# Kernel tuning notes

Hardware: AMD Instinct MI355X
Metric: run time of the kernel (lower is better)

## Reference

```python
import jax, jax.numpy as jnp
import numpy as np

B, S, HID = 2, 2048, 1024
NH, NKV, HD = 16, 8, 128
EPS = 1e-6
THETA = 1.0e6
NEG = -1e9

def _rope_tables():
    inv_freq = 1.0 / (THETA ** (np.arange(0, HD, 2, dtype=np.float32) / HD))  # [HD/2]
    pos = np.arange(S, dtype=np.float32)
    freqs = np.outer(pos, inv_freq)                      # [S, HD/2]
    emb = np.concatenate([freqs, freqs], axis=-1)        # [S, HD]
    cos = np.broadcast_to(np.cos(emb), (B, S, HD)).copy()
    sin = np.broadcast_to(np.sin(emb), (B, S, HD)).copy()
    return jnp.asarray(cos), jnp.asarray(sin)

def setup_inputs() -> dict:
    key = jax.random.key(0)
    ks = jax.random.split(key, 8)
    hidden_states = jax.random.normal(ks[0], (B, S, HID), jnp.float32)
    cos, sin = _rope_tables()
    # additive causal mask [B,1,S,S]
    causal = jnp.triu(jnp.full((S, S), NEG, jnp.float32), k=1)
    attention_mask = jnp.broadcast_to(causal[None, None], (B, 1, S, S))
    std = 0.02
    Wq = jax.random.normal(ks[1], (NH * HD, HID), jnp.float32) * std
    Wk = jax.random.normal(ks[2], (NKV * HD, HID), jnp.float32) * std
    Wv = jax.random.normal(ks[3], (NKV * HD, HID), jnp.float32) * std
    Wo = jax.random.normal(ks[4], (HID, NH * HD), jnp.float32) * std
    q_norm_w = jnp.ones((HD,), jnp.float32)
    k_norm_w = jnp.ones((HD,), jnp.float32)
    return {"hidden_states": hidden_states, "cos": cos, "sin": sin,
            "attention_mask": attention_mask, "Wq": Wq, "Wk": Wk, "Wv": Wv,
            "Wo": Wo, "q_norm_w": q_norm_w, "k_norm_w": k_norm_w}

def _rms_norm(x, w):
    var = jnp.mean(jnp.square(x), axis=-1, keepdims=True)
    return x * jax.lax.rsqrt(var + EPS) * w

def _rotate_half(x):
    x1, x2 = jnp.split(x, 2, axis=-1)
    return jnp.concatenate([-x2, x1], axis=-1)

def reference(hidden_states, cos, sin, attention_mask, Wq, Wk, Wv, Wo, q_norm_w, k_norm_w):
    # projections: [B,S,heads,HD] -> [B,heads,S,HD]
    q = jnp.einsum('bsh,dh->bsd', hidden_states, Wq).reshape(B, S, NH, HD)
    k = jnp.einsum('bsh,dh->bsd', hidden_states, Wk).reshape(B, S, NKV, HD)
    v = jnp.einsum('bsh,dh->bsd', hidden_states, Wv).reshape(B, S, NKV, HD)
    q = jnp.transpose(_rms_norm(q, q_norm_w), (0, 2, 1, 3))
    k = jnp.transpose(_rms_norm(k, k_norm_w), (0, 2, 1, 3))
    v = jnp.transpose(v, (0, 2, 1, 3))
    c = cos[:, None]  # [B,1,S,HD]
    s = sin[:, None]
    q = q * c + _rotate_half(q) * s
    k = k * c + _rotate_half(k) * s
    # repeat kv heads: NKV -> NH
    n_rep = NH // NKV
    k = jnp.repeat(k, n_rep, axis=1)
    v = jnp.repeat(v, n_rep, axis=1)
    scaling = HD ** -0.5
    scores = jnp.einsum('bhqd,bhkd->bhqk', q, k) * scaling
    scores = scores + attention_mask
    probs = jax.nn.softmax(scores.astype(jnp.float32), axis=-1).astype(q.dtype)
    out = jnp.einsum('bhqk,bhkd->bhqd', probs, v)
    out = jnp.transpose(out, (0, 2, 1, 3)).reshape(B, S, NH * HD)
    return jnp.einsum('bsd,hd->bsh', out, Wo)
```

## Files before the change

### kernel.cpp

```cpp
#include <hip/hip_runtime.h>
#include <hip/hip_fp16.h>


typedef _Float16 f16;
typedef __attribute__((ext_vector_type(8))) _Float16 f16x8;
typedef __attribute__((ext_vector_type(4))) _Float16 f16x4;
typedef __attribute__((ext_vector_type(4))) float f32x4;

__constant__ const float kEps = 1e-6f;
__constant__ const float kScaleL2 = 0.1275179120685481f;

#define ASYNC_LD16(gp, lp)                                              \
  __builtin_amdgcn_global_load_lds(                                     \
      (const __attribute__((address_space(1))) void*)(gp),              \
      (__attribute__((address_space(3))) void*)(uint32_t)(uintptr_t)(lp), 16, 0, 0)

__device__ __forceinline__ float dpp_max16(float v) {
  int x;
  x = __builtin_amdgcn_update_dpp(0, __builtin_bit_cast(int, v), 0xB1, 0xF, 0xF, true);
  v = fmaxf(v, __builtin_bit_cast(float, x));
  x = __builtin_amdgcn_update_dpp(0, __builtin_bit_cast(int, v), 0x4E, 0xF, 0xF, true);
  v = fmaxf(v, __builtin_bit_cast(float, x));
  x = __builtin_amdgcn_update_dpp(0, __builtin_bit_cast(int, v), 0x141, 0xF, 0xF, true);
  v = fmaxf(v, __builtin_bit_cast(float, x));
  x = __builtin_amdgcn_update_dpp(0, __builtin_bit_cast(int, v), 0x140, 0xF, 0xF, true);
  v = fmaxf(v, __builtin_bit_cast(float, x));
  return v;
}
__device__ __forceinline__ float dpp_sum16(float v) {
  int x;
  x = __builtin_amdgcn_update_dpp(0, __builtin_bit_cast(int, v), 0xB1, 0xF, 0xF, true);
  v += __builtin_bit_cast(float, x);
  x = __builtin_amdgcn_update_dpp(0, __builtin_bit_cast(int, v), 0x4E, 0xF, 0xF, true);
  v += __builtin_bit_cast(float, x);
  x = __builtin_amdgcn_update_dpp(0, __builtin_bit_cast(int, v), 0x141, 0xF, 0xF, true);
  v += __builtin_bit_cast(float, x);
  x = __builtin_amdgcn_update_dpp(0, __builtin_bit_cast(int, v), 0x140, 0xF, 0xF, true);
  v += __builtin_bit_cast(float, x);
  return v;
}

__global__ __launch_bounds__(256) void cast_f32_f16(const float* __restrict__ in,
                                                    f16* __restrict__ out, int n) {
  int i = (blockIdx.x * 256 + threadIdx.x) * 4;
  if (i >= n) return;
  f32x4 v = *reinterpret_cast<const f32x4*>(in + i);
  f16x4 o;
  o.x = (f16)v.x; o.y = (f16)v.y; o.z = (f16)v.z; o.w = (f16)v.w;
  *reinterpret_cast<f16x4*>(out + i) = o;
}

__global__ __launch_bounds__(256) void gemm_bt(const f16* __restrict__ A,
                                               const f16* __restrict__ Bm,
                                               float* __restrict__ C,
                                               int M, int N, int K) {
  __shared__ __align__(16) f16 As[128][64];
  __shared__ __align__(16) f16 Bs[128][64];
  const int tid = threadIdx.x;
  const int lane = tid & 63;
  const int wave = tid >> 6;
  const int cl = lane & 15;
  const int quad = lane >> 4;
  const int wm = (wave >> 1) * 64;
  const int wn = (wave & 1) * 64;
  const int tm = blockIdx.y * 128;
  const int tn = blockIdx.x * 128;
  const int r0 = tid >> 3;
  const int csw = ((tid & 7) ^ (r0 & 7)) * 8;

  const f16* Ab = A + (size_t)(tm + r0) * K + csw;
  const f16* Bb = Bm + (size_t)(tn + r0) * K + csw;
  char* Al = (char*)As + wave * 1024;
  char* Bl = (char*)Bs + wave * 1024;

  f32x4 acc[4][4] = {};

  for (int k0 = 0; k0 < K; k0 += 64) {
#pragma unroll
    for (int c = 0; c < 4; ++c) {
      ASYNC_LD16(Ab + (size_t)(c * 32) * K + k0, Al + c * 4096);
      ASYNC_LD16(Bb + (size_t)(c * 32) * K + k0, Bl + c * 4096);
    }
    __syncthreads();
#pragma unroll
    for (int kk = 0; kk < 2; ++kk) {
      f16x8 af[4], bf[4];
#pragma unroll
      for (int mi = 0; mi < 4; ++mi)
        af[mi] = *reinterpret_cast<const f16x8*>(
            &As[wm + mi * 16 + cl][((kk * 4 + quad) ^ (cl & 7)) * 8]);
#pragma unroll
      for (int ni = 0; ni < 4; ++ni)
        bf[ni] = *reinterpret_cast<const f16x8*>(
            &Bs[wn + ni * 16 + cl][((kk * 4 + quad) ^ (cl & 7)) * 8]);
#pragma unroll
      for (int mi = 0; mi < 4; ++mi)
#pragma unroll
        for (int ni = 0; ni < 4; ++ni)
          acc[mi][ni] =
              __builtin_amdgcn_mfma_f32_16x16x32_f16(af[mi], bf[ni], acc[mi][ni], 0, 0, 0);
    }
    __syncthreads();
  }
#pragma unroll
  for (int mi = 0; mi < 4; ++mi)
#pragma unroll
    for (int ni = 0; ni < 4; ++ni)
#pragma unroll
      for (int r = 0; r < 4; ++r)
        C[(size_t)(tm + wm + mi * 16 + quad * 4 + r) * N + tn + wn + ni * 16 + cl] =
            acc[mi][ni][r];
}

__global__ __launch_bounds__(256) void rope_norm(
    const float* __restrict__ qkvf,
    const float* __restrict__ cosT, const float* __restrict__ sinT,
    const float* __restrict__ qw, const float* __restrict__ kw,
    f16* __restrict__ qt, f16* __restrict__ kt) {
  const int gw = blockIdx.x * 4 + (threadIdx.x >> 6);
  const int lane = threadIdx.x & 63;
  const int head = gw % 24;
  const int bs = gw / 24;
  const bool isq = head < 16;
  const float* src = qkvf + (size_t)bs * 4096 +
                     (isq ? head * 128 : 2048 + (head - 16) * 128);
  const float x1 = src[lane];
  const float x2 = src[lane + 64];
  float ss = x1 * x1 + x2 * x2;
#pragma unroll
  for (int off = 32; off >= 1; off >>= 1) ss += __shfl_xor(ss, off);
  const float rms = rsqrtf(ss * (1.0f / 128.0f) + kEps);
  const float* w = isq ? qw : kw;
  const float n1 = x1 * rms * w[lane];
  const float n2 = x2 * rms * w[lane + 64];
  const float* cb = cosT + (size_t)bs * 128;
  const float* sb = sinT + (size_t)bs * 128;
  const float o1 = n1 * cb[lane] - n2 * sb[lane];
  const float o2 = n2 * cb[lane + 64] + n1 * sb[lane + 64];
  const int b = bs >> 11;
  const int s = bs & 2047;
  f16* dst;
  float sc;
  if (isq) {
    dst = qt + ((size_t)(b * 16 + head) * 2048 + s) * 128;
    sc = kScaleL2;
  } else {
    dst = kt + ((size_t)(b * 8 + (head - 16)) * 2048 + s) * 128;
    sc = 1.0f;
  }
  dst[lane] = (f16)(o1 * sc);
  dst[lane + 64] = (f16)(o2 * sc);
}

__global__ __launch_bounds__(256) void v_transpose(const float* __restrict__ qkvf,
                                                   f16* __restrict__ vt) {
  __shared__ f16 tile[64][136];
  const int bh = blockIdx.y;
  const int b = bh >> 3, h = bh & 7;
  const int s0 = blockIdx.x * 64;
  const int tid = threadIdx.x;
#pragma unroll
  for (int i = 0; i < 8; ++i) {
    int c = tid + i * 256;
    int s = c >> 5;
    int d0 = (c & 31) * 4;
    f32x4 v = *reinterpret_cast<const f32x4*>(
        qkvf + (size_t)(b * 2048 + s0 + s) * 4096 + 3072 + h * 128 + d0);
    tile[s][d0 + 0] = (f16)v.x;
    tile[s][d0 + 1] = (f16)v.y;
    tile[s][d0 + 2] = (f16)v.z;
    tile[s][d0 + 3] = (f16)v.w;
  }
  __syncthreads();
#pragma unroll
  for (int i = 0; i < 4; ++i) {
    int c = tid + i * 256;
    int d = c >> 3;
    int sB = (c & 7) * 8;
    f16x8 o;
#pragma unroll
    for (int j = 0; j < 8; ++j) o[j] = tile[sB + j][d];
    *reinterpret_cast<f16x8*>(vt + ((size_t)(b * 8 + h) * 128 + d) * 2048 + s0 + sB) = o;
  }
}

__global__ __launch_bounds__(128) void attn(const f16* __restrict__ Qt,
                                            const f16* __restrict__ Kt,
                                            const f16* __restrict__ Vt,
                                            f16* __restrict__ Ot) {
  __shared__ __align__(16) f16 Ks[64][136];
  __shared__ __align__(16) f16 Vs[128][72];
  __shared__ __align__(16) f16 Ps[2][32][72];

  const int bid = blockIdx.x;
  const int bh = bid & 31;
  const int t = 31 - (bid >> 5);
  const int q0 = t * 64;
  const int b = bh >> 4, h = bh & 15;
  const int kv = h >> 1;

  const int tid = threadIdx.x;
  const int lane = tid & 63, wv = tid >> 6;
  const int cl = lane & 15, quad = lane >> 4;

  const f16* qbase = Qt + ((size_t)(b * 16 + h) * 2048 + q0 + wv * 32 + cl) * 128;
  f16x8 aq[2][4];
#pragma unroll
  for (int mi = 0; mi < 2; ++mi)
#pragma unroll
    for (int kk = 0; kk < 4; ++kk)
      aq[mi][kk] =
          *reinterpret_cast<const f16x8*>(qbase + mi * 16 * 128 + kk * 32 + quad * 8);

  const f16* kbase = Kt + (size_t)(b * 8 + kv) * 2048 * 128;
  const f16* vbase = Vt + (size_t)(b * 8 + kv) * 128 * 2048;

  float m_[2][4], l_[2][4];
#pragma unroll
  for (int mi = 0; mi < 2; ++mi)
#pragma unroll
    for (int r = 0; r < 4; ++r) { m_[mi][r] = -1e30f; l_[mi][r] = 0.f; }
  f32x4 oacc[2][8] = {};

  for (int kt0 = 0; kt0 <= q0; kt0 += 64) {
#pragma unroll
    for (int i = 0; i < 8; ++i) {
      int c = tid + i * 128;
      int krow = c >> 4, d0 = (c & 15) * 8;
      *reinterpret_cast<int4*>(&Ks[krow][d0]) =
          *reinterpret_cast<const int4*>(kbase + (size_t)(kt0 + krow) * 128 + d0);
      int dr = c >> 3, ko = (c & 7) * 8;
      *reinterpret_cast<int4*>(&Vs[dr][ko]) =
          *reinterpret_cast<const int4*>(vbase + (size_t)dr * 2048 + kt0 + ko);
    }
    __syncthreads();
    f32x4 sacc[2][4] = {};
#pragma unroll
    for (int kk = 0; kk < 4; ++kk)
#pragma unroll
      for (int ni = 0; ni < 4; ++ni) {
        f16x8 bk = *reinterpret_cast<const f16x8*>(&Ks[ni * 16 + cl][kk * 32 + quad * 8]);
#pragma unroll
        for (int mi = 0; mi < 2; ++mi)
          sacc[mi][ni] =
              __builtin_amdgcn_mfma_f32_16x16x32_f16(aq[mi][kk], bk, sacc[mi][ni], 0, 0, 0);
      }
    if (kt0 == q0) {
#pragma unroll
      for (int mi = 0; mi < 2; ++mi) {
        const int qr = wv * 32 + mi * 16 + quad * 4;
#pragma unroll
        for (int ni = 0; ni < 4; ++ni) {
          const int kg = ni * 16 + cl;
#pragma unroll
          for (int r = 0; r < 4; ++r)
            if (kg > qr + r) sacc[mi][ni][r] = -1e30f;
        }
      }
    }
    float alv[2][4];
#pragma unroll
    for (int mi = 0; mi < 2; ++mi)
#pragma unroll
      for (int r = 0; r < 4; ++r) {
        float mx = fmaxf(fmaxf(sacc[mi][0][r], sacc[mi][1][r]),
                         fmaxf(sacc[mi][2][r], sacc[mi][3][r]));
        mx = dpp_max16(mx);
        const float nm = fmaxf(m_[mi][r], mx);
        const float al = __builtin_amdgcn_exp2f(m_[mi][r] - nm);
        m_[mi][r] = nm;
        float ps = 0.f;
#pragma unroll
        for (int ni = 0; ni < 4; ++ni) {
          const float p = __builtin_amdgcn_exp2f(sacc[mi][ni][r] - nm);
          sacc[mi][ni][r] = p;
          ps += p;
        }
        l_[mi][r] = l_[mi][r] * al + ps;
        alv[mi][r] = al;
      }
#pragma unroll
    for (int mi = 0; mi < 2; ++mi)
#pragma unroll
      for (int ni = 0; ni < 4; ++ni)
#pragma unroll
        for (int r = 0; r < 4; ++r)
          Ps[wv][mi * 16 + quad * 4 + r][ni * 16 + cl] = (f16)sacc[mi][ni][r];
#pragma unroll
    for (int mi = 0; mi < 2; ++mi)
#pragma unroll
      for (int dg = 0; dg < 8; ++dg)
#pragma unroll
        for (int r = 0; r < 4; ++r) oacc[mi][dg][r] *= alv[mi][r];
    asm volatile("s_waitcnt lgkmcnt(0)" ::: "memory");
    f16x8 ap[2][2];
#pragma unroll
    for (int mi = 0; mi < 2; ++mi)
#pragma unroll
      for (int kh = 0; kh < 2; ++kh)
        ap[mi][kh] =
            *reinterpret_cast<const f16x8*>(&Ps[wv][mi * 16 + cl][kh * 32 + quad * 8]);
#pragma unroll
    for (int kh = 0; kh < 2; ++kh)
#pragma unroll
      for (int dg = 0; dg < 8; ++dg) {
        f16x8 bv = *reinterpret_cast<const f16x8*>(&Vs[dg * 16 + cl][kh * 32 + quad * 8]);
#pragma unroll
        for (int mi = 0; mi < 2; ++mi)
          oacc[mi][dg] =
              __builtin_amdgcn_mfma_f32_16x16x32_f16(ap[mi][kh], bv, oacc[mi][dg], 0, 0, 0);
      }
    __syncthreads();
  }
#pragma unroll
  for (int mi = 0; mi < 2; ++mi)
#pragma unroll
    for (int r = 0; r < 4; ++r) {
      const float inv = 1.0f / dpp_sum16(l_[mi][r]);
      const int qg = q0 + wv * 32 + mi * 16 + quad * 4 + r;
#pragma unroll
      for (int dg = 0; dg < 8; ++dg)
        Ot[(size_t)(b * 2048 + qg) * 2048 + h * 128 + dg * 16 + cl] =
            (f16)(oacc[mi][dg][r] * inv);
    }
}

extern "C" void kernel_launch(void* const* d_in, const int* in_sizes, int n_in,
                              void* d_out, int out_size, void* d_ws, size_t ws_size,
                              hipStream_t stream) {
  (void)in_sizes; (void)n_in; (void)out_size; (void)ws_size;
  const float* hidden = (const float*)d_in[0];
  const float* cosT = (const float*)d_in[1];
  const float* sinT = (const float*)d_in[2];
  const float* Wq = (const float*)d_in[4];
  const float* Wk = (const float*)d_in[5];
  const float* Wv = (const float*)d_in[6];
  const float* Wo = (const float*)d_in[7];
  const float* qnw = (const float*)d_in[8];
  const float* knw = (const float*)d_in[9];
  float* out = (float*)d_out;

  char* ws = (char*)d_ws;
  size_t off = 0;
  auto alloc = [&](size_t bytes) {
    char* p = ws + off;
    off += (bytes + 255) & ~(size_t)255;
    return p;
  };
  f16* hb = (f16*)alloc(4096ull * 1024 * 2);
  f16* wqkv = (f16*)alloc(4096ull * 1024 * 2);
  f16* wob = (f16*)alloc(1024ull * 2048 * 2);
  float* qkvf = (float*)alloc(4096ull * 4096 * 4);
  f16* qt = (f16*)alloc(32ull * 2048 * 128 * 2);
  f16* kt = (f16*)alloc(16ull * 2048 * 128 * 2);
  f16* vt = (f16*)alloc(16ull * 2048 * 128 * 2);
  f16* ot = (f16*)alloc(4096ull * 2048 * 2);

  cast_f32_f16<<<4096, 256, 0, stream>>>(hidden, hb, 4194304);
  cast_f32_f16<<<2048, 256, 0, stream>>>(Wq, wqkv, 2097152);
  cast_f32_f16<<<1024, 256, 0, stream>>>(Wk, wqkv + 2048ull * 1024, 1048576);
  cast_f32_f16<<<1024, 256, 0, stream>>>(Wv, wqkv + 3072ull * 1024, 1048576);
  cast_f32_f16<<<2048, 256, 0, stream>>>(Wo, wob, 2097152);

  gemm_bt<<<dim3(32, 32), 256, 0, stream>>>(hb, wqkv, qkvf, 4096, 4096, 1024);

  rope_norm<<<24576, 256, 0, stream>>>(qkvf, cosT, sinT, qnw, knw, qt, kt);
  v_transpose<<<dim3(32, 16), 256, 0, stream>>>(qkvf, vt);

  attn<<<1024, 128, 0, stream>>>(qt, kt, vt, ot);

  gemm_bt<<<dim3(8, 32), 256, 0, stream>>>(ot, wob, out, 4096, 1024, 2048);
}
```

Before: 326.2 us.

## Fuse casts, store QKV as fp16, retile output GEMM to 64-row blocks

Merges the five fp32-to-fp16 cast launches into one kernel. The QKV projection now writes fp16 instead of fp32, which halves the intermediate buffer that rope_norm and v_transpose read back; v_transpose now loads with 16-byte vector loads. The output projection uses a new 64x128-tile GEMM so 512 blocks launch instead of 256, filling more compute units. Keeping QKV in fp16 before the RMS norm costs some precision on the pre-norm activations.

```diff
diff --git a/kernel.cpp b/kernel.cpp
--- a/kernel.cpp
+++ b/kernel.cpp
@@ -40,20 +40,31 @@
   return v;
 }
 
-__global__ __launch_bounds__(256) void cast_f32_f16(const float* __restrict__ in,
-                                                    f16* __restrict__ out, int n) {
-  int i = (blockIdx.x * 256 + threadIdx.x) * 4;
-  if (i >= n) return;
-  f32x4 v = *reinterpret_cast<const f32x4*>(in + i);
+__global__ __launch_bounds__(256) void cast_all(
+    const float* __restrict__ h, const float* __restrict__ wq,
+    const float* __restrict__ wk, const float* __restrict__ wv,
+    const float* __restrict__ wo, f16* __restrict__ hb,
+    f16* __restrict__ wqkv, f16* __restrict__ wob) {
+  const int idx = blockIdx.x * 256 + threadIdx.x;
+  const float* src;
+  f16* dst;
+  int base;
+  if (idx < 1048576) { src = h;  dst = hb;                  base = 0; }
+  else if (idx < 1572864) { src = wq; dst = wqkv;               base = 1048576; }
+  else if (idx < 1835008) { src = wk; dst = wqkv + 2048 * 1024; base = 1572864; }
+  else if (idx < 2097152) { src = wv; dst = wqkv + 3072 * 1024; base = 1835008; }
+  else { src = wo; dst = wob; base = 2097152; }
+  const int i = (idx - base) * 4;
+  f32x4 v = *reinterpret_cast<const f32x4*>(src + i);
   f16x4 o;
   o.x = (f16)v.x; o.y = (f16)v.y; o.z = (f16)v.z; o.w = (f16)v.w;
-  *reinterpret_cast<f16x4*>(out + i) = o;
-}
-
-__global__ __launch_bounds__(256) void gemm_bt(const f16* __restrict__ A,
-                                               const f16* __restrict__ Bm,
-                                               float* __restrict__ C,
-                                               int M, int N, int K) {
+  *reinterpret_cast<f16x4*>(dst + i) = o;
+}
+
+__global__ __launch_bounds__(256) void gemm_bt_h(const f16* __restrict__ A,
+                                                 const f16* __restrict__ Bm,
+                                                 f16* __restrict__ C,
+                                                 int M, int N, int K) {
   __shared__ __align__(16) f16 As[128][64];
   __shared__ __align__(16) f16 Bs[128][64];
   const int tid = threadIdx.x;
@@ -109,11 +120,74 @@
 #pragma unroll
       for (int r = 0; r < 4; ++r)
         C[(size_t)(tm + wm + mi * 16 + quad * 4 + r) * N + tn + wn + ni * 16 + cl] =
+            (f16)acc[mi][ni][r];
+}
+
+__global__ __launch_bounds__(256) void gemm_bt64(const f16* __restrict__ A,
+                                                 const f16* __restrict__ Bm,
+                                                 float* __restrict__ C,
+                                                 int M, int N, int K) {
+  __shared__ __align__(16) f16 As[64][64];
+  __shared__ __align__(16) f16 Bs[128][64];
+  const int tid = threadIdx.x;
+  const int lane = tid & 63;
+  const int wave = tid >> 6;
+  const int cl = lane & 15;
+  const int quad = lane >> 4;
+  const int wm = (wave >> 1) * 32;
+  const int wn = (wave & 1) * 64;
+  const int tm = blockIdx.y * 64;
+  const int tn = blockIdx.x * 128;
+  const int r0 = tid >> 3;
+  const int csw = ((tid & 7) ^ (r0 & 7)) * 8;
+
+  const f16* Ab = A + (size_t)(tm + r0) * K + csw;
+  const f16* Bb = Bm + (size_t)(tn + r0) * K + csw;
+  char* Al = (char*)As + wave * 1024;
+  char* Bl = (char*)Bs + wave * 1024;
+
+  f32x4 acc[2][4] = {};
+
+  for (int k0 = 0; k0 < K; k0 += 64) {
+#pragma unroll
+    for (int c = 0; c < 2; ++c)
+      ASYNC_LD16(Ab + (size_t)(c * 32) * K + k0, Al + c * 4096);
+#pragma unroll
+    for (int c = 0; c < 4; ++c)
+      ASYNC_LD16(Bb + (size_t)(c * 32) * K + k0, Bl + c * 4096);
+    __syncthreads();
+#pragma unroll
+    for (int kk = 0; kk < 2; ++kk) {
+      f16x8 af[2], bf[4];
+#pragma unroll
+      for (int mi = 0; mi < 2; ++mi)
+        af[mi] = *reinterpret_cast<const f16x8*>(
+            &As[wm + mi * 16 + cl][((kk * 4 + quad) ^ (cl & 7)) * 8]);
+#pragma unroll
+      for (int ni = 0; ni < 4; ++ni)
+        bf[ni] = *reinterpret_cast<const f16x8*>(
+            &Bs[wn + ni * 16 + cl][((kk * 4 + quad) ^ (cl & 7)) * 8]);
+#pragma unroll
+      for (int mi = 0; mi < 2; ++mi)
+#pragma unroll
+        for (int ni = 0; ni < 4; ++ni)
+          acc[mi][ni] =
+              __builtin_amdgcn_mfma_f32_16x16x32_f16(af[mi], bf[ni], acc[mi][ni], 0, 0, 0);
+    }
+    __syncthreads();
+  }
+#pragma unroll
+  for (int mi = 0; mi < 2; ++mi)
+#pragma unroll
+    for (int ni = 0; ni < 4; ++ni)
+#pragma unroll
+      for (int r = 0; r < 4; ++r)
+        C[(size_t)(tm + wm + mi * 16 + quad * 4 + r) * N + tn + wn + ni * 16 + cl] =
             acc[mi][ni][r];
 }
 
 __global__ __launch_bounds__(256) void rope_norm(
-    const float* __restrict__ qkvf,
+    const f16* __restrict__ qkvh,
     const float* __restrict__ cosT, const float* __restrict__ sinT,
     const float* __restrict__ qw, const float* __restrict__ kw,
     f16* __restrict__ qt, f16* __restrict__ kt) {
@@ -122,10 +196,10 @@
   const int head = gw % 24;
   const int bs = gw / 24;
   const bool isq = head < 16;
-  const float* src = qkvf + (size_t)bs * 4096 +
-                     (isq ? head * 128 : 2048 + (head - 16) * 128);
-  const float x1 = src[lane];
-  const float x2 = src[lane + 64];
+  const f16* src = qkvh + (size_t)bs * 4096 +
+                   (isq ? head * 128 : 2048 + (head - 16) * 128);
+  const float x1 = (float)src[lane];
+  const float x2 = (float)src[lane + 64];
   float ss = x1 * x1 + x2 * x2;
 #pragma unroll
   for (int off = 32; off >= 1; off >>= 1) ss += __shfl_xor(ss, off);
@@ -152,24 +226,21 @@
   dst[lane + 64] = (f16)(o2 * sc);
 }
 
-__global__ __launch_bounds__(256) void v_transpose(const float* __restrict__ qkvf,
+__global__ __launch_bounds__(256) void v_transpose(const f16* __restrict__ qkvh,
                                                    f16* __restrict__ vt) {
-  __shared__ f16 tile[64][136];
+  __shared__ __align__(16) f16 tile[64][136];
   const int bh = blockIdx.y;
   const int b = bh >> 3, h = bh & 7;
   const int s0 = blockIdx.x * 64;
   const int tid = threadIdx.x;
 #pragma unroll
-  for (int i = 0; i < 8; ++i) {
+  for (int i = 0; i < 4; ++i) {
     int c = tid + i * 256;
-    int s = c >> 5;
-    int d0 = (c & 31) * 4;
-    f32x4 v = *reinterpret_cast<const f32x4*>(
-        qkvf + (size_t)(b * 2048 + s0 + s) * 4096 + 3072 + h * 128 + d0);
-    tile[s][d0 + 0] = (f16)v.x;
-    tile[s][d0 + 1] = (f16)v.y;
-    tile[s][d0 + 2] = (f16)v.z;
-    tile[s][d0 + 3] = (f16)v.w;
+    int s = c >> 4;
+    int cg = c & 15;
+    f16x8 v = *reinterpret_cast<const f16x8*>(
+        qkvh + (size_t)(b * 2048 + s0 + s) * 4096 + 3072 + h * 128 + cg * 8);
+    *reinterpret_cast<f16x8*>(&tile[s][cg * 8]) = v;
   }
   __syncthreads();
 #pragma unroll
@@ -350,24 +421,20 @@
   f16* hb = (f16*)alloc(4096ull * 1024 * 2);
   f16* wqkv = (f16*)alloc(4096ull * 1024 * 2);
   f16* wob = (f16*)alloc(1024ull * 2048 * 2);
-  float* qkvf = (float*)alloc(4096ull * 4096 * 4);
+  f16* qkvh = (f16*)alloc(4096ull * 4096 * 2);
   f16* qt = (f16*)alloc(32ull * 2048 * 128 * 2);
   f16* kt = (f16*)alloc(16ull * 2048 * 128 * 2);
   f16* vt = (f16*)alloc(16ull * 2048 * 128 * 2);
   f16* ot = (f16*)alloc(4096ull * 2048 * 2);
 
-  cast_f32_f16<<<4096, 256, 0, stream>>>(hidden, hb, 4194304);
-  cast_f32_f16<<<2048, 256, 0, stream>>>(Wq, wqkv, 2097152);
-  cast_f32_f16<<<1024, 256, 0, stream>>>(Wk, wqkv + 2048ull * 1024, 1048576);
-  cast_f32_f16<<<1024, 256, 0, stream>>>(Wv, wqkv + 3072ull * 1024, 1048576);
-  cast_f32_f16<<<2048, 256, 0, stream>>>(Wo, wob, 2097152);
-
-  gemm_bt<<<dim3(32, 32), 256, 0, stream>>>(hb, wqkv, qkvf, 4096, 4096, 1024);
-
-  rope_norm<<<24576, 256, 0, stream>>>(qkvf, cosT, sinT, qnw, knw, qt, kt);
-  v_transpose<<<dim3(32, 16), 256, 0, stream>>>(qkvf, vt);
+  cast_all<<<10240, 256, 0, stream>>>(hidden, Wq, Wk, Wv, Wo, hb, wqkv, wob);
+
+  gemm_bt_h<<<dim3(32, 32), 256, 0, stream>>>(hb, wqkv, qkvh, 4096, 4096, 1024);
+
+  rope_norm<<<24576, 256, 0, stream>>>(qkvh, cosT, sinT, qnw, knw, qt, kt);
+  v_transpose<<<dim3(32, 16), 256, 0, stream>>>(qkvh, vt);
 
   attn<<<1024, 128, 0, stream>>>(qt, kt, vt, ot);
 
-  gemm_bt<<<dim3(8, 32), 256, 0, stream>>>(ot, wob, out, 4096, 1024, 2048);
-}
+  gemm_bt64<<<dim3(8, 64), 256, 0, stream>>>(ot, wob, out, 4096, 1024, 2048);
+}
```

Result: faster. 316.3 us (-3.0%).
